# Performance work log

Hardware: AMD Instinct MI355X
Metric: run time of the kernel (lower is better)

## Reference

```python
import jax, jax.numpy as jnp
import numpy as np


def setup_inputs() -> dict:
    key = jax.random.key(0)
    ks = jax.random.split(key, 18)
    B, T, L, C = 16, 512, 50, 7
    H = 512
    s = 0.05
    inp = {
        "phone_data": jax.random.normal(ks[0], (B, T, L, C), jnp.float32),
        "h0": jax.random.normal(ks[1], (B, H), jnp.float32),
        "conv1_w": jax.random.normal(ks[2], (128, 7, 11), jnp.float32) * s,
        "conv1_b": jax.random.normal(ks[3], (128,), jnp.float32) * s,
        "conv2_w": jax.random.normal(ks[4], (256, 128, 9), jnp.float32) * s,
        "conv2_b": jax.random.normal(ks[5], (256,), jnp.float32) * s,
        "fc1_w": jax.random.normal(ks[6], (1024, 1536), jnp.float32) * s,
        "fc1_b": jax.random.normal(ks[7], (1024,), jnp.float32) * s,
        "fc2_w": jax.random.normal(ks[8], (512, 1024), jnp.float32) * s,
        "fc2_b": jax.random.normal(ks[9], (512,), jnp.float32) * s,
        "gru_wih": jax.random.normal(ks[10], (3 * H, H), jnp.float32) * s,
        "gru_whh": jax.random.normal(ks[11], (3 * H, H), jnp.float32) * s,
        "gru_bih": jax.random.normal(ks[12], (3 * H,), jnp.float32) * s,
        "gru_bhh": jax.random.normal(ks[13], (3 * H,), jnp.float32) * s,
        "fc3_w": jax.random.normal(ks[14], (1, H), jnp.float32) * s,
        "fc3_b": jax.random.normal(ks[15], (1,), jnp.float32) * s,
    }
    return inp


def reference(phone_data, h0, conv1_w, conv1_b, conv2_w, conv2_b,
              fc1_w, fc1_b, fc2_w, fc2_b,
              gru_wih, gru_whh, gru_bih, gru_bhh, fc3_w, fc3_b):
    B, T, L, C = phone_data.shape
    N = B * T
    # ---- batched CNN + FC feature extractor (independent per frame) ----
    x = phone_data.reshape(N, L, C).transpose(0, 2, 1)  # [N, 7, 50]
    y = jax.lax.conv_general_dilated(
        x, conv1_w, (1,), 'VALID',
        dimension_numbers=('NCH', 'OIH', 'NCH')) + conv1_b[None, :, None]  # [N,128,40]
    y = y.reshape(N, 128, 20, 2).max(-1)  # maxpool k=2,s=2 -> [N,128,20]
    y = jax.lax.conv_general_dilated(
        y, conv2_w, (1,), 'VALID',
        dimension_numbers=('NCH', 'OIH', 'NCH')) + conv2_b[None, :, None]  # [N,256,12]
    y = y.reshape(N, 256, 6, 2).max(-1)  # [N,256,6]
    feat = y.reshape(N, 1536)            # Flatten(0): channel-major, matches torch
    feat = feat @ fc1_w.T + fc1_b        # [N,1024]
    feat = feat @ fc2_w.T + fc2_b        # [N,512]
    feat = feat.reshape(B, T, 512)

    # ---- sequential GRUCell recurrence (PyTorch GRUCell math) ----
    def cell(h, x_t):
        gi = x_t @ gru_wih.T + gru_bih   # [B, 3H]
        gh = h @ gru_whh.T + gru_bhh     # [B, 3H]
        ir, iz, in_ = jnp.split(gi, 3, axis=-1)
        hr, hz, hn = jnp.split(gh, 3, axis=-1)
        r = jax.nn.sigmoid(ir + hr)
        z = jax.nn.sigmoid(iz + hz)
        n = jnp.tanh(in_ + r * hn)
        h_new = (1 - z) * n + z * h
        # original code calls hx.detach() every step
        h_new = jax.lax.stop_gradient(h_new)
        return h_new, h_new

    _, hs = jax.lax.scan(cell, h0, feat.transpose(1, 0, 2))  # hs: [T,B,512]
    out = hs @ fc3_w.T + fc3_b  # [T,B,1]
    return out.transpose(1, 0, 2)  # [B,T,1]
```

## Files before the change

### kernel.cpp

```cpp
#include <hip/hip_runtime.h>
#include <hip/hip_bf16.h>
#include <math.h>
#include <stdint.h>

typedef __attribute__((ext_vector_type(8))) short short8;
typedef __attribute__((ext_vector_type(4))) float f32x4;
typedef __attribute__((ext_vector_type(4))) unsigned int uint4v;

#define T_ 512

__device__ __forceinline__ unsigned short bf16rn(float f) {
  union { float f; unsigned u; } x; x.f = f;
  unsigned r = x.u + 0x7FFF + ((x.u >> 16) & 1);
  return (unsigned short)(r >> 16);
}

__device__ __forceinline__ void gload16(const void* gsrc, void* ldst) {
  __builtin_amdgcn_global_load_lds(
      (const __attribute__((address_space(1))) unsigned int*)gsrc,
      (__attribute__((address_space(3))) unsigned int*)ldst, 16, 0, 0);
}

__device__ __forceinline__ void wg_barrier() {
  __builtin_amdgcn_sched_barrier(0);
  asm volatile("s_waitcnt lgkmcnt(0)" ::: "memory");
  __builtin_amdgcn_sched_barrier(0);
  __builtin_amdgcn_s_barrier();
  __builtin_amdgcn_sched_barrier(0);
}

__global__ __launch_bounds__(256) void conv1_kernel(
    const float* __restrict__ phone, const float* __restrict__ w1,
    const float* __restrict__ b1, ushort* __restrict__ out1b) {
  __shared__ float ws[128 * 77];
  __shared__ float bs[128];
  __shared__ float xs[8][7][52];
  const int tid = threadIdx.x;
  const int n0 = blockIdx.x * 8;
  for (int idx = tid; idx < 9856; idx += 256) ws[idx] = w1[idx];
  if (tid < 128) bs[tid] = b1[tid];
  for (int idx = tid; idx < 2800; idx += 256) {
    int fi = idx / 350, r = idx - fi * 350;
    int ll = r / 7, c = r - ll * 7;
    xs[fi][c][ll] = phone[(size_t)(n0 + fi) * 350 + r];
  }
  __syncthreads();

  const int o = tid >> 1, ph = tid & 1;
  const float* wo = ws + o * 77;
  const float bb = bs[o];
  for (int fi = 0; fi < 8; ++fi) {
    float acc0[10], acc1[10];
#pragma unroll
    for (int q = 0; q < 10; ++q) { acc0[q] = 0.f; acc1[q] = 0.f; }
    for (int i = 0; i < 7; ++i) {
      float wr[11];
#pragma unroll
      for (int k = 0; k < 11; ++k) wr[k] = wo[i * 11 + k];
#pragma unroll
      for (int q = 0; q < 10; ++q) {
        int p = ph * 10 + q;
        int base = 2 * p;
        float xv[12];
#pragma unroll
        for (int j = 0; j < 12; ++j) xv[j] = xs[fi][i][base + j];
        float s0 = 0.f, s1 = 0.f;
#pragma unroll
        for (int k = 0; k < 11; ++k) {
          s0 += xv[k] * wr[k];
          s1 += xv[k + 1] * wr[k];
        }
        acc0[q] += s0;
        acc1[q] += s1;
      }
    }
#pragma unroll
    for (int q = 0; q < 10; ++q) {
      int p = ph * 10 + q;
      out1b[((size_t)(n0 + fi) * 128 + o) * 20 + p] =
          bf16rn(fmaxf(acc0[q], acc1[q]) + bb);
    }
  }
}

__global__ __launch_bounds__(256) void f32_to_bf16_multi(
    const float* __restrict__ s0, ushort* __restrict__ d0,
    const float* __restrict__ s1, ushort* __restrict__ d1,
    const float* __restrict__ s2, ushort* __restrict__ d2,
    const float* __restrict__ s3, ushort* __restrict__ d3) {
  const int n0 = 73728, n1 = 393216, n2 = 131072, n3 = 196608;
  int i = blockIdx.x * 256 + threadIdx.x;
  const float* s; ushort* d; int off;
  if (i < n0) { s = s0; d = d0; off = i; }
  else if (i < n0 + n1) { s = s1; d = d1; off = i - n0; }
  else if (i < n0 + n1 + n2) { s = s2; d = d2; off = i - n0 - n1; }
  else if (i < n0 + n1 + n2 + n3) { s = s3; d = d3; off = i - n0 - n1 - n2; }
  else return;
  float4 v = ((const float4*)s)[off];
  ushort4 o;
  o.x = bf16rn(v.x); o.y = bf16rn(v.y); o.z = bf16rn(v.z); o.w = bf16rn(v.w);
  ((ushort4*)d)[off] = o;
}

__global__ __launch_bounds__(256) void stage_h0(
    const float* __restrict__ h0, unsigned long long* __restrict__ hxt) {
  const int tid = threadIdx.x;
#pragma unroll
  for (int k = 0; k < 16; ++k) {
    int idx = tid + k * 256;
    int g = idx >> 10, rem = idx & 1023;
    int s = rem >> 6, w = rem & 63;
    int b4 = (w >> 2) & 3, fqk = w >> 4, p2 = w & 3;
    int b = g * 4 + b4;
    int D = s * 32 + fqk * 8 + p2 * 2;
    float2 h2 = *(const float2*)(h0 + (size_t)b * 512 + D);
    unsigned pk = (unsigned)bf16rn(h2.x) | ((unsigned)bf16rn(h2.y) << 16);
    hxt[(size_t)g * 2048 + rem] = (unsigned long long)pk;
  }
}

template <int AM, int EM>
__global__ __launch_bounds__(256) void gemm_bf16(
    const ushort* __restrict__ A, const ushort* __restrict__ W,
    const float* __restrict__ bias, void* __restrict__ Cout,
    int K, int lda, int ldc) {
  __shared__ ushort As[128 * 64];
  __shared__ ushort Bs[128 * 64];
  __shared__ ushort tbl[1152];
  const int tid = threadIdx.x;
  const int l = tid & 63, wv = tid >> 6;
  const int wr = wv >> 1, wc = wv & 1;
  const int fr = l & 15, fq = l >> 4;
  const int bm0 = blockIdx.x * 128, bn0 = blockIdx.y * 128;

  if (AM == 1) {
    for (int idx = tid; idx < 1152; idx += 256) {
      int i2 = idx / 9, kp = idx - i2 * 9;
      tbl[idx] = (ushort)(i2 * 20 + kp);
    }
    __syncthreads();
  }

  f32x4 acc[4][4];
#pragma unroll
  for (int mi = 0; mi < 4; ++mi)
#pragma unroll
    for (int ni = 0; ni < 4; ++ni) acc[mi][ni] = (f32x4)0.f;

  const int pr8 = l >> 3;
  const int pc = l & 7;
  const int nkt = K >> 6;
  for (int kt = 0; kt < nkt; ++kt) {
    const int k0 = kt << 6;
#pragma unroll
    for (int i = 0; i < 4; ++i) {
      int q = wv * 4 + i;
      int prow = q * 8 + pr8;
      int lc = pc ^ (prow & 7);
      gload16(W + (size_t)(bn0 + prow) * K + k0 + lc * 8, &Bs[q * 512]);
    }
    if (AM == 0) {
#pragma unroll
      for (int i = 0; i < 4; ++i) {
        int q = wv * 4 + i;
        int prow = q * 8 + pr8;
        int lc = pc ^ (prow & 7);
        gload16(A + (size_t)(bm0 + prow) * lda + k0 + lc * 8, &As[q * 512]);
      }
    } else {
#pragma unroll
      for (int q = 0; q < 16; ++q) {
        int idx = tid + q * 256;
        int row = idx >> 5, c0 = (idx & 31) * 2;
        int m = bm0 + row;
        int n = m / 12, pos = m - n * 12;
        int kk = k0 + c0;
        const ushort* an = A + (size_t)n * 2560 + pos;
        uint e0 = an[tbl[kk]];
        uint e1 = an[tbl[kk + 1]];
        *(uint*)&As[row * 64 + (((c0 >> 3) ^ (row & 7)) << 3) + (c0 & 7)] =
            e0 | (e1 << 16);
      }
    }
    __syncthreads();
#pragma unroll
    for (int ks = 0; ks < 2; ++ks) {
      short8 af[4], bfr[4];
#pragma unroll
      for (int mi = 0; mi < 4; ++mi) {
        int row = wr * 64 + mi * 16 + fr;
        af[mi] = *(const short8*)&As[row * 64 + (((ks * 4 + fq) ^ (row & 7)) << 3)];
      }
#pragma unroll
      for (int ni = 0; ni < 4; ++ni) {
        int row = wc * 64 + ni * 16 + fr;
        bfr[ni] = *(const short8*)&Bs[row * 64 + (((ks * 4 + fq) ^ (row & 7)) << 3)];
      }
#pragma unroll
      for (int mi = 0; mi < 4; ++mi)
#pragma unroll
        for (int ni = 0; ni < 4; ++ni)
          acc[mi][ni] = __builtin_amdgcn_mfma_f32_16x16x32_bf16(
              af[mi], bfr[ni], acc[mi][ni], 0, 0, 0);
    }
    __syncthreads();
  }

#pragma unroll
  for (int ni = 0; ni < 4; ++ni) {
    int col = bn0 + wc * 64 + ni * 16 + fr;
    float bv = bias[col];
#pragma unroll
    for (int mi = 0; mi < 4; ++mi) {
      int mbase = bm0 + wr * 64 + mi * 16 + fq * 4;
      if (EM == 0) {
        ushort* C = (ushort*)Cout;
#pragma unroll
        for (int j = 0; j < 4; ++j)
          C[(size_t)(mbase + j) * ldc + col] = bf16rn(acc[mi][ni][j] + bv);
      } else if (EM == 1) {
        ushort* C = (ushort*)Cout;
#pragma unroll
        for (int j = 0; j < 4; j += 2) {
          int m = mbase + j;
          int n = m / 12, pos = m - n * 12;
          float v = fmaxf(acc[mi][ni][j], acc[mi][ni][j + 1]) + bv;
          C[(size_t)n * 1536 + col * 6 + (pos >> 1)] = bf16rn(v);
        }
      } else {
        float* C = (float*)Cout;
#pragma unroll
        for (int j = 0; j < 4; ++j) {
          int m = mbase + j;
          int b = m >> 9, tt = m & 511;
          C[((size_t)tt * 16 + b) * 1536 + col] = acc[mi][ni][j] + bv;
        }
      }
    }
  }
}

__global__ __launch_bounds__(512) void gru_persistent(
    const float* __restrict__ h0, const float* __restrict__ gi,
    const float* __restrict__ whh, const float* __restrict__ bhh,
    float* __restrict__ hsbuf, unsigned long long* __restrict__ hxt) {
  __shared__ float gh_lds[24 * 64];
  __shared__ unsigned afl[16 * 64 * 4];
  const int tid = threadIdx.x;
  const int g = blockIdx.x >> 2, wp = blockIdx.x & 3;
  const int l = tid & 63, v = tid >> 6;
  const int fr = l & 15, fq = l >> 4;
  unsigned long long* hxg = hxt + (size_t)g * 2048;

  for (int i = tid; i < 4096; i += 512) afl[i] = 0u;

  const int tA = 3 * v, tB = 3 * v + 1, tC = 3 * v + 2;
  const int oA = (tA >> 3) * 512 + wp * 128 + (tA & 7) * 16 + fr;
  const int oB = (tB >> 3) * 512 + wp * 128 + (tB & 7) * 16 + fr;
  const int oC = (tC >> 3) * 512 + wp * 128 + (tC & 7) * 16 + fr;
  short8 bfA[16], bfB[16], bfC[16];
#pragma unroll
  for (int s = 0; s < 16; ++s) {
    const float* pA = whh + (size_t)oA * 512 + s * 32 + fq * 8;
    const float* pB = whh + (size_t)oB * 512 + s * 32 + fq * 8;
    const float* pC = whh + (size_t)oC * 512 + s * 32 + fq * 8;
    float4 a0 = *(const float4*)pA, a1 = *(const float4*)(pA + 4);
    float4 b0 = *(const float4*)pB, b1 = *(const float4*)(pB + 4);
    float4 c0 = *(const float4*)pC, c1 = *(const float4*)(pC + 4);
    short8 x, y, z;
    x[0] = (short)bf16rn(a0.x); x[1] = (short)bf16rn(a0.y);
    x[2] = (short)bf16rn(a0.z); x[3] = (short)bf16rn(a0.w);
    x[4] = (short)bf16rn(a1.x); x[5] = (short)bf16rn(a1.y);
    x[6] = (short)bf16rn(a1.z); x[7] = (short)bf16rn(a1.w);
    y[0] = (short)bf16rn(b0.x); y[1] = (short)bf16rn(b0.y);
    y[2] = (short)bf16rn(b0.z); y[3] = (short)bf16rn(b0.w);
    y[4] = (short)bf16rn(b1.x); y[5] = (short)bf16rn(b1.y);
    y[6] = (short)bf16rn(b1.z); y[7] = (short)bf16rn(b1.w);
    z[0] = (short)bf16rn(c0.x); z[1] = (short)bf16rn(c0.y);
    z[2] = (short)bf16rn(c0.z); z[3] = (short)bf16rn(c0.w);
    z[4] = (short)bf16rn(c1.x); z[5] = (short)bf16rn(c1.y);
    z[6] = (short)bf16rn(c1.z); z[7] = (short)bf16rn(c1.w);
    bfA[s] = x; bfB[s] = y; bfC[s] = z;
  }
  const float boA = bhh[oA], boB = bhh[oB], boC = bhh[oC];

  const int b4 = tid >> 6, jp = tid & 63, jl = jp * 2;
  const bool gthr = (tid < 256);
  const bool pthr = (tid >= 256 && tid < 384);
  const int pt = tid - 256;
  const int bglob = g * 4 + (b4 & 3);
  const int jglob = wp * 128 + jl;
  float hA = 0.f, hB = 0.f;
  float giC0 = 0.f, giC1 = 0.f, giC2 = 0.f, giC3 = 0.f, giC4 = 0.f, giC5 = 0.f;
  float giN0 = 0.f, giN1 = 0.f, giN2 = 0.f, giN3 = 0.f, giN4 = 0.f, giN5 = 0.f;
  if (gthr) {
    float2 h2 = *(const float2*)(h0 + (size_t)bglob * 512 + jglob);
    hA = h2.x; hB = h2.y;
    const float* g0 = gi + (size_t)bglob * 1536 + jglob;
    float2 r0 = *(const float2*)(g0);
    float2 r1 = *(const float2*)(g0 + 512);
    float2 r2 = *(const float2*)(g0 + 1024);
    giC0 = r0.x; giC3 = r0.y; giC1 = r1.x; giC4 = r1.y; giC2 = r2.x; giC5 = r2.y;
    const float* g1 = gi + (size_t)(16 + bglob) * 1536 + jglob;
    float2 s0 = *(const float2*)(g1);
    float2 s1 = *(const float2*)(g1 + 512);
    float2 s2 = *(const float2*)(g1 + 1024);
    giN0 = s0.x; giN3 = s0.y; giN1 = s1.x; giN4 = s1.y; giN2 = s2.x; giN5 = s2.y;
  }
  __syncthreads();

  if (pthr) {
    const int ps = pt >> 3;
    const int w0 = (pt & 7) * 8;
    const unsigned long long* base = hxg + ps * 64 + w0;
    uint4v r[4];
    for (;;) {
#pragma unroll
      for (int q = 0; q < 4; ++q)
        asm volatile("global_load_dwordx4 %0, %1, off sc0 sc1"
                     : "=v"(r[q]) : "v"(base + q * 2));
      asm volatile("s_waitcnt vmcnt(0)" ::: "memory");
      __builtin_amdgcn_sched_barrier(0);
      bool ok = true;
#pragma unroll
      for (int q = 0; q < 4; ++q)
        ok = ok & (r[q].y == 0u) & (r[q].w == 0u);
      if (ok) break;
    }
#pragma unroll
    for (int q = 0; q < 4; ++q) {
      int w = w0 + 2 * q;
      int lane = ((w >> 2) & 3) | ((w >> 4) << 4);
      *(uint2*)&afl[(ps * 64 + lane) * 4 + (w & 3)] = make_uint2(r[q].x, r[q].z);
    }
  }
  wg_barrier();

  for (int t = 0; t < T_; ++t) {
    f32x4 aA = (f32x4)0.f, aB = (f32x4)0.f, aC = (f32x4)0.f;
#pragma unroll
    for (int s = 0; s < 16; ++s) {
      union { uint4v u; short8 s8; } ca;
      ca.u = *(const uint4v*)&afl[(s * 64 + l) * 4];
      aA = __builtin_amdgcn_mfma_f32_16x16x32_bf16(ca.s8, bfA[s], aA, 0, 0, 0);
      aB = __builtin_amdgcn_mfma_f32_16x16x32_bf16(ca.s8, bfB[s], aB, 0, 0, 0);
      aC = __builtin_amdgcn_mfma_f32_16x16x32_bf16(ca.s8, bfC[s], aC, 0, 0, 0);
    }
    if (fq == 0) {
#pragma unroll
      for (int j = 0; j < 4; ++j) {
        gh_lds[tA * 64 + j * 16 + fr] = aA[j] + boA;
        gh_lds[tB * 64 + j * 16 + fr] = aB[j] + boB;
        gh_lds[tC * 64 + j * 16 + fr] = aC[j] + boC;
      }
    }
    wg_barrier();

    if (gthr) {
      const int tl = jl >> 4, c = jl & 15;
      float2 rr = *(const float2*)&gh_lds[(0 + tl) * 64 + b4 * 16 + c];
      float2 zz = *(const float2*)&gh_lds[(8 + tl) * 64 + b4 * 16 + c];
      float2 nn = *(const float2*)&gh_lds[(16 + tl) * 64 + b4 * 16 + c];
      float rgA = __builtin_amdgcn_rcpf(1.f + __expf(-(giC0 + rr.x)));
      float rgB = __builtin_amdgcn_rcpf(1.f + __expf(-(giC3 + rr.y)));
      float zgA = __builtin_amdgcn_rcpf(1.f + __expf(-(giC1 + zz.x)));
      float zgB = __builtin_amdgcn_rcpf(1.f + __expf(-(giC4 + zz.y)));
      float eA = __expf(2.f * (giC2 + rgA * nn.x));
      float eB = __expf(2.f * (giC5 + rgB * nn.y));
      float ngA = 1.f - 2.f * __builtin_amdgcn_rcpf(eA + 1.f);
      float ngB = 1.f - 2.f * __builtin_amdgcn_rcpf(eB + 1.f);
      hA = (1.f - zgA) * ngA + zgA * hA;
      hB = (1.f - zgB) * ngB + zgB * hB;
      if (t + 1 < T_) {
        unsigned pk = (unsigned)bf16rn(hA) | ((unsigned)bf16rn(hB) << 16);
        unsigned long long payload =
            (unsigned long long)pk | ((unsigned long long)(unsigned)(t + 1) << 32);
        int s = wp * 4 + (jl >> 5);
        int w_i = (((jl >> 3) & 3) * 4 + b4) * 4 + ((jl & 7) >> 1);
        __hip_atomic_store(hxg + ((t + 1) & 1) * 1024 + s * 64 + w_i, payload,
                           __ATOMIC_RELAXED, __HIP_MEMORY_SCOPE_AGENT);
      }
      *(float2*)(hsbuf + ((size_t)t * 16 + bglob) * 512 + jglob) =
          make_float2(hA, hB);
      giC0 = giN0; giC1 = giN1; giC2 = giN2;
      giC3 = giN3; giC4 = giN4; giC5 = giN5;
      if (t + 2 < T_) {
        const float* gb = gi + ((size_t)(t + 2) * 16 + bglob) * 1536 + jglob;
        float2 r0 = *(const float2*)(gb);
        float2 r1 = *(const float2*)(gb + 512);
        float2 r2 = *(const float2*)(gb + 1024);
        giN0 = r0.x; giN3 = r0.y; giN1 = r1.x; giN4 = r1.y; giN2 = r2.x; giN5 = r2.y;
      }
    } else if (pthr && t + 1 < T_) {
      const int ps = pt >> 3;
      const int w0 = (pt & 7) * 8;
      const unsigned long long* base =
          hxg + ((t + 1) & 1) * 1024 + ps * 64 + w0;
      const unsigned tag = (unsigned)(t + 1);
      uint4v r[4];
      for (;;) {
#pragma unroll
        for (int q = 0; q < 4; ++q)
          asm volatile("global_load_dwordx4 %0, %1, off sc0 sc1"
                       : "=v"(r[q]) : "v"(base + q * 2));
        asm volatile("s_waitcnt vmcnt(0)" ::: "memory");
        __builtin_amdgcn_sched_barrier(0);
        bool ok = true;
#pragma unroll
        for (int q = 0; q < 4; ++q)
          ok = ok & (r[q].y == tag) & (r[q].w == tag);
        if (ok) break;
      }
#pragma unroll
      for (int q = 0; q < 4; ++q) {
        int w = w0 + 2 * q;
        int lane = ((w >> 2) & 3) | ((w >> 4) << 4);
        *(uint2*)&afl[(ps * 64 + lane) * 4 + (w & 3)] = make_uint2(r[q].x, r[q].z);
      }
    }
    wg_barrier();
  }
}

__global__ __launch_bounds__(256) void fc3_kernel(
    const float* __restrict__ hs, const float* __restrict__ w3,
    const float* __restrict__ b3, float* __restrict__ out) {
  __shared__ float w[512];
  const int tid = threadIdx.x;
  w[tid] = w3[tid];
  w[tid + 256] = w3[tid + 256];
  __syncthreads();
  const int gidx = blockIdx.x * 256 + tid;
  const int b = gidx >> 9, t = gidx & 511;
  const float4* hr = (const float4*)(hs + ((size_t)t * 16 + b) * 512);
  const float4* wr = (const float4*)w;
  float acc = 0.f;
#pragma unroll 8
  for (int kc = 0; kc < 128; ++kc) {
    float4 h = hr[kc], ww = wr[kc];
    acc += h.x * ww.x + h.y * ww.y + h.z * ww.z + h.w * ww.w;
  }
  out[gidx] = acc + b3[0];
}

extern "C" void kernel_launch(void* const* d_in, const int* in_sizes, int n_in,
                              void* d_out, int out_size, void* d_ws,
                              size_t ws_size, hipStream_t stream) {
  const float* phone = (const float*)d_in[0];
  const float* h0    = (const float*)d_in[1];
  const float* w1    = (const float*)d_in[2];
  const float* b1    = (const float*)d_in[3];
  const float* w2    = (const float*)d_in[4];
  const float* b2    = (const float*)d_in[5];
  const float* fc1w  = (const float*)d_in[6];
  const float* fc1b  = (const float*)d_in[7];
  const float* fc2w  = (const float*)d_in[8];
  const float* fc2b  = (const float*)d_in[9];
  const float* wih   = (const float*)d_in[10];
  const float* whh   = (const float*)d_in[11];
  const float* bih   = (const float*)d_in[12];
  const float* bhh   = (const float*)d_in[13];
  const float* w3    = (const float*)d_in[14];
  const float* b3    = (const float*)d_in[15];
  float* out = (float*)d_out;

  char* ws = (char*)d_ws;
  ushort* out1b = (ushort*)(ws + 0);
  ushort* feat2 = (ushort*)(ws + 41943040);
  ushort* feat3 = (ushort*)(ws + 67108864);
  ushort* feat4 = (ushort*)(ws + 83886080);
  float*  gibuf = (float*) (ws + 92274688);
  float*  hsbuf = (float*) (ws + 142606336);
  ushort* w2b   = (ushort*)(ws + 159383552);
  ushort* fc1wb = (ushort*)(ws + 159973376);
  ushort* fc2wb = (ushort*)(ws + 163119104);
  ushort* wihb  = (ushort*)(ws + 164167680);
  unsigned long long* hxt = (unsigned long long*)(ws + 67108864);

  f32_to_bf16_multi<<<3104, 256, 0, stream>>>(w2, w2b, fc1w, fc1wb,
                                              fc2w, fc2wb, wih, wihb);

  conv1_kernel<<<1024, 256, 0, stream>>>(phone, w1, b1, out1b);
  gemm_bf16<1, 1><<<dim3(768, 2), 256, 0, stream>>>(out1b, w2b, b2, feat2, 1152, 0, 0);
  gemm_bf16<0, 0><<<dim3(64, 8), 256, 0, stream>>>(feat2, fc1wb, fc1b, feat3, 1536, 1536, 1024);
  gemm_bf16<0, 0><<<dim3(64, 4), 256, 0, stream>>>(feat3, fc2wb, fc2b, feat4, 1024, 1024, 512);
  gemm_bf16<0, 2><<<dim3(64, 12), 256, 0, stream>>>(feat4, wihb, bih, gibuf, 512, 512, 1536);

  hipMemsetAsync(hxt, 0, 65536, stream);
  stage_h0<<<1, 256, 0, stream>>>(h0, hxt);
  gru_persistent<<<16, 512, 0, stream>>>(h0, gibuf, whh, bhh, hsbuf, hxt);

  fc3_kernel<<<32, 256, 0, stream>>>(hsbuf, w3, b3, out);
}
```

Baseline: 1.529 ms.

## Restructure persistent GRU: gate-aligned MFMA tiles, double-buffered LDS, one barrier per step

Each GRU block now handles 8 batches and 64 hidden units. Every wave computes the r, z and n tiles for the same hidden indices, so the gate math runs directly on MFMA accumulators. This removes the gh_lds round-trip and one workgroup barrier per timestep. The h-vector LDS buffer is double-buffered and fed by dedicated poller waves, the initial h0 is staged in-kernel so the stage_h0 launch is dropped, and the block shrinks to 384 threads. The trade-off is that half the lanes do gate work, and the cross-block exchange now spans 8 blocks per group instead of 4.

Result: slower. 1.893 ms (+23.8%).

```diff
diff --git a/kernel.cpp b/kernel.cpp
--- a/kernel.cpp
+++ b/kernel.cpp
@@ -102,23 +102,6 @@
   ((ushort4*)d)[off] = o;
 }
 
-__global__ __launch_bounds__(256) void stage_h0(
-    const float* __restrict__ h0, unsigned long long* __restrict__ hxt) {
-  const int tid = threadIdx.x;
-#pragma unroll
-  for (int k = 0; k < 16; ++k) {
-    int idx = tid + k * 256;
-    int g = idx >> 10, rem = idx & 1023;
-    int s = rem >> 6, w = rem & 63;
-    int b4 = (w >> 2) & 3, fqk = w >> 4, p2 = w & 3;
-    int b = g * 4 + b4;
-    int D = s * 32 + fqk * 8 + p2 * 2;
-    float2 h2 = *(const float2*)(h0 + (size_t)b * 512 + D);
-    unsigned pk = (unsigned)bf16rn(h2.x) | ((unsigned)bf16rn(h2.y) << 16);
-    hxt[(size_t)g * 2048 + rem] = (unsigned long long)pk;
-  }
-}
-
 template <int AM, int EM>
 __global__ __launch_bounds__(256) void gemm_bf16(
     const ushort* __restrict__ A, const ushort* __restrict__ W,
@@ -240,33 +223,75 @@
   }
 }
 
-__global__ __launch_bounds__(512) void gru_persistent(
+__global__ __launch_bounds__(384) void gru_persistent(
     const float* __restrict__ h0, const float* __restrict__ gi,
     const float* __restrict__ whh, const float* __restrict__ bhh,
     float* __restrict__ hsbuf, unsigned long long* __restrict__ hxt) {
-  __shared__ float gh_lds[24 * 64];
-  __shared__ unsigned afl[16 * 64 * 4];
+  __shared__ unsigned afl[2][4096];
   const int tid = threadIdx.x;
-  const int g = blockIdx.x >> 2, wp = blockIdx.x & 3;
+  const int g = blockIdx.x >> 3, wp = blockIdx.x & 7;
   const int l = tid & 63, v = tid >> 6;
   const int fr = l & 15, fq = l >> 4;
-  unsigned long long* hxg = hxt + (size_t)g * 2048;
-
-  for (int i = tid; i < 4096; i += 512) afl[i] = 0u;
-
-  const int tA = 3 * v, tB = 3 * v + 1, tC = 3 * v + 2;
-  const int oA = (tA >> 3) * 512 + wp * 128 + (tA & 7) * 16 + fr;
-  const int oB = (tB >> 3) * 512 + wp * 128 + (tB & 7) * 16 + fr;
-  const int oC = (tC >> 3) * 512 + wp * 128 + (tC & 7) * 16 + fr;
-  short8 bfA[16], bfB[16], bfC[16];
+  unsigned long long* hxg = hxt + (size_t)g * 4096;
+
+  for (int i = tid; i < 2048; i += 384) {
+    int s = i >> 7, w_i = i & 127;
+    int p2 = w_i & 3, idx2 = w_i >> 2;
+    int b8 = idx2 & 7, fqk = idx2 >> 3;
+    int Dd = s * 32 + fqk * 8 + p2 * 2;
+    float2 h2 = *(const float2*)(h0 + (size_t)(g * 8 + b8) * 512 + Dd);
+    unsigned pk = (unsigned)bf16rn(h2.x) | ((unsigned)bf16rn(h2.y) << 16);
+    afl[0][(s * 64 + b8 + 16 * fqk) * 4 + p2] = pk;
+  }
+
+  if (v >= 4) {
+    const int pt = tid - 256;
+    const int ps = pt >> 3;
+    const int pw0 = (pt & 7) * 2;
+    __syncthreads();
+    for (int t = 0; t < T_; ++t) {
+      if (t + 1 < T_) {
+        const unsigned long long* base =
+            hxg + (size_t)((t + 1) & 1) * 2048 + ps * 128;
+        const unsigned tag = (unsigned)(t + 1);
+        unsigned* dst = afl[(t + 1) & 1];
+        uint4v r[8];
+        for (;;) {
+#pragma unroll
+          for (int q = 0; q < 8; ++q)
+            asm volatile("global_load_dwordx4 %0, %1, off sc0 sc1"
+                         : "=v"(r[q]) : "v"(base + pw0 + q * 16));
+          asm volatile("s_waitcnt vmcnt(0)" ::: "memory");
+          __builtin_amdgcn_sched_barrier(0);
+          bool ok = true;
+#pragma unroll
+          for (int q = 0; q < 8; ++q)
+            ok = ok & (r[q].y == tag) & (r[q].w == tag);
+          if (ok) break;
+        }
+#pragma unroll
+        for (int q = 0; q < 8; ++q) {
+          int w_i = pw0 + q * 16;
+          int lane = ((w_i >> 2) & 7) + 16 * (w_i >> 5);
+          *(uint2*)&dst[(ps * 64 + lane) * 4 + (w_i & 3)] =
+              make_uint2(r[q].x, r[q].z);
+        }
+      }
+      wg_barrier();
+    }
+    return;
+  }
+
+  const int D = wp * 64 + v * 16 + fr;
+  short8 bfR[16], bfZ[16], bfN[16];
 #pragma unroll
   for (int s = 0; s < 16; ++s) {
-    const float* pA = whh + (size_t)oA * 512 + s * 32 + fq * 8;
-    const float* pB = whh + (size_t)oB * 512 + s * 32 + fq * 8;
-    const float* pC = whh + (size_t)oC * 512 + s * 32 + fq * 8;
-    float4 a0 = *(const float4*)pA, a1 = *(const float4*)(pA + 4);
-    float4 b0 = *(const float4*)pB, b1 = *(const float4*)(pB + 4);
-    float4 c0 = *(const float4*)pC, c1 = *(const float4*)(pC + 4);
+    const float* pR = whh + (size_t)(0 * 512 + D) * 512 + s * 32 + fq * 8;
+    const float* pZ = whh + (size_t)(1 * 512 + D) * 512 + s * 32 + fq * 8;
+    const float* pN = whh + (size_t)(2 * 512 + D) * 512 + s * 32 + fq * 8;
+    float4 a0 = *(const float4*)pR, a1 = *(const float4*)(pR + 4);
+    float4 b0 = *(const float4*)pZ, b1 = *(const float4*)(pZ + 4);
+    float4 c0 = *(const float4*)pN, c1 = *(const float4*)(pN + 4);
     short8 x, y, z;
     x[0] = (short)bf16rn(a0.x); x[1] = (short)bf16rn(a0.y);
     x[2] = (short)bf16rn(a0.z); x[3] = (short)bf16rn(a0.w);
@@ -280,142 +305,81 @@
     z[2] = (short)bf16rn(c0.z); z[3] = (short)bf16rn(c0.w);
     z[4] = (short)bf16rn(c1.x); z[5] = (short)bf16rn(c1.y);
     z[6] = (short)bf16rn(c1.z); z[7] = (short)bf16rn(c1.w);
-    bfA[s] = x; bfB[s] = y; bfC[s] = z;
-  }
-  const float boA = bhh[oA], boB = bhh[oB], boC = bhh[oC];
-
-  const int b4 = tid >> 6, jp = tid & 63, jl = jp * 2;
-  const bool gthr = (tid < 256);
-  const bool pthr = (tid >= 256 && tid < 384);
-  const int pt = tid - 256;
-  const int bglob = g * 4 + (b4 & 3);
-  const int jglob = wp * 128 + jl;
-  float hA = 0.f, hB = 0.f;
-  float giC0 = 0.f, giC1 = 0.f, giC2 = 0.f, giC3 = 0.f, giC4 = 0.f, giC5 = 0.f;
-  float giN0 = 0.f, giN1 = 0.f, giN2 = 0.f, giN3 = 0.f, giN4 = 0.f, giN5 = 0.f;
-  if (gthr) {
-    float2 h2 = *(const float2*)(h0 + (size_t)bglob * 512 + jglob);
-    hA = h2.x; hB = h2.y;
-    const float* g0 = gi + (size_t)bglob * 1536 + jglob;
-    float2 r0 = *(const float2*)(g0);
-    float2 r1 = *(const float2*)(g0 + 512);
-    float2 r2 = *(const float2*)(g0 + 1024);
-    giC0 = r0.x; giC3 = r0.y; giC1 = r1.x; giC4 = r1.y; giC2 = r2.x; giC5 = r2.y;
-    const float* g1 = gi + (size_t)(16 + bglob) * 1536 + jglob;
-    float2 s0 = *(const float2*)(g1);
-    float2 s1 = *(const float2*)(g1 + 512);
-    float2 s2 = *(const float2*)(g1 + 1024);
-    giN0 = s0.x; giN3 = s0.y; giN1 = s1.x; giN4 = s1.y; giN2 = s2.x; giN5 = s2.y;
+    bfR[s] = x; bfZ[s] = y; bfN[s] = z;
+  }
+  const float boR = bhh[D], boZ = bhh[512 + D], boN = bhh[1024 + D];
+
+  const bool glane = (fq < 2);
+  float h[4];
+  float gR[4], gZ[4], gN_[4], nR[4], nZ[4], nN_[4];
+  if (glane) {
+#pragma unroll
+    for (int j = 0; j < 4; ++j) {
+      int bg = g * 8 + fq * 4 + j;
+      h[j] = h0[(size_t)bg * 512 + D];
+      const float* p0 = gi + (size_t)bg * 1536 + D;
+      gR[j] = p0[0]; gZ[j] = p0[512]; gN_[j] = p0[1024];
+      const float* p1 = gi + (size_t)(16 + bg) * 1536 + D;
+      nR[j] = p1[0]; nZ[j] = p1[512]; nN_[j] = p1[1024];
+    }
   }
   __syncthreads();
 
-  if (pthr) {
-    const int ps = pt >> 3;
-    const int w0 = (pt & 7) * 8;
-    const unsigned long long* base = hxg + ps * 64 + w0;
-    uint4v r[4];
-    for (;;) {
-#pragma unroll
-      for (int q = 0; q < 4; ++q)
-        asm volatile("global_load_dwordx4 %0, %1, off sc0 sc1"
-                     : "=v"(r[q]) : "v"(base + q * 2));
-      asm volatile("s_waitcnt vmcnt(0)" ::: "memory");
-      __builtin_amdgcn_sched_barrier(0);
-      bool ok = true;
-#pragma unroll
-      for (int q = 0; q < 4; ++q)
-        ok = ok & (r[q].y == 0u) & (r[q].w == 0u);
-      if (ok) break;
-    }
-#pragma unroll
-    for (int q = 0; q < 4; ++q) {
-      int w = w0 + 2 * q;
-      int lane = ((w >> 2) & 3) | ((w >> 4) << 4);
-      *(uint2*)&afl[(ps * 64 + lane) * 4 + (w & 3)] = make_uint2(r[q].x, r[q].z);
-    }
-  }
-  wg_barrier();
+  const int s_f = D >> 5;
+  const int wbase = (((D >> 3) & 3) * 8 + fq * 4) * 4 + ((D & 7) >> 1);
 
   for (int t = 0; t < T_; ++t) {
-    f32x4 aA = (f32x4)0.f, aB = (f32x4)0.f, aC = (f32x4)0.f;
+    const unsigned* ab = afl[t & 1];
+    f32x4 aR = (f32x4)0.f, aZ = (f32x4)0.f, aN = (f32x4)0.f;
 #pragma unroll
     for (int s = 0; s < 16; ++s) {
       union { uint4v u; short8 s8; } ca;
-      ca.u = *(const uint4v*)&afl[(s * 64 + l) * 4];
-      aA = __builtin_amdgcn_mfma_f32_16x16x32_bf16(ca.s8, bfA[s], aA, 0, 0, 0);
-      aB = __builtin_amdgcn_mfma_f32_16x16x32_bf16(ca.s8, bfB[s], aB, 0, 0, 0);
-      aC = __builtin_amdgcn_mfma_f32_16x16x32_bf16(ca.s8, bfC[s], aC, 0, 0, 0);
-    }
-    if (fq == 0) {
+      ca.u = *(const uint4v*)&ab[(s * 64 + l) * 4];
+      aR = __builtin_amdgcn_mfma_f32_16x16x32_bf16(ca.s8, bfR[s], aR, 0, 0, 0);
+      aZ = __builtin_amdgcn_mfma_f32_16x16x32_bf16(ca.s8, bfZ[s], aZ, 0, 0, 0);
+      aN = __builtin_amdgcn_mfma_f32_16x16x32_bf16(ca.s8, bfN[s], aN, 0, 0, 0);
+    }
+    if (glane) {
+      unsigned myh[4];
 #pragma unroll
       for (int j = 0; j < 4; ++j) {
-        gh_lds[tA * 64 + j * 16 + fr] = aA[j] + boA;
-        gh_lds[tB * 64 + j * 16 + fr] = aB[j] + boB;
-        gh_lds[tC * 64 + j * 16 + fr] = aC[j] + boC;
-      }
-    }
-    wg_barrier();
-
-    if (gthr) {
-      const int tl = jl >> 4, c = jl & 15;
-      float2 rr = *(const float2*)&gh_lds[(0 + tl) * 64 + b4 * 16 + c];
-      float2 zz = *(const float2*)&gh_lds[(8 + tl) * 64 + b4 * 16 + c];
-      float2 nn = *(const float2*)&gh_lds[(16 + tl) * 64 + b4 * 16 + c];
-      float rgA = __builtin_amdgcn_rcpf(1.f + __expf(-(giC0 + rr.x)));
-      float rgB = __builtin_amdgcn_rcpf(1.f + __expf(-(giC3 + rr.y)));
-      float zgA = __builtin_amdgcn_rcpf(1.f + __expf(-(giC1 + zz.x)));
-      float zgB = __builtin_amdgcn_rcpf(1.f + __expf(-(giC4 + zz.y)));
-      float eA = __expf(2.f * (giC2 + rgA * nn.x));
-      float eB = __expf(2.f * (giC5 + rgB * nn.y));
-      float ngA = 1.f - 2.f * __builtin_amdgcn_rcpf(eA + 1.f);
-      float ngB = 1.f - 2.f * __builtin_amdgcn_rcpf(eB + 1.f);
-      hA = (1.f - zgA) * ngA + zgA * hA;
-      hB = (1.f - zgB) * ngB + zgB * hB;
+        float rr = aR[j] + boR, zz = aZ[j] + boZ, nn = aN[j] + boN;
+        float rg = __builtin_amdgcn_rcpf(1.f + __expf(-(gR[j] + rr)));
+        float zg = __builtin_amdgcn_rcpf(1.f + __expf(-(gZ[j] + zz)));
+        float e = __expf(2.f * (gN_[j] + rg * nn));
+        float ng = 1.f - 2.f * __builtin_amdgcn_rcpf(e + 1.f);
+        h[j] = (1.f - zg) * ng + zg * h[j];
+        myh[j] = (unsigned)bf16rn(h[j]);
+      }
       if (t + 1 < T_) {
-        unsigned pk = (unsigned)bf16rn(hA) | ((unsigned)bf16rn(hB) << 16);
-        unsigned long long payload =
-            (unsigned long long)pk | ((unsigned long long)(unsigned)(t + 1) << 32);
-        int s = wp * 4 + (jl >> 5);
-        int w_i = (((jl >> 3) & 3) * 4 + b4) * 4 + ((jl & 7) >> 1);
-        __hip_atomic_store(hxg + ((t + 1) & 1) * 1024 + s * 64 + w_i, payload,
-                           __ATOMIC_RELAXED, __HIP_MEMORY_SCOPE_AGENT);
-      }
-      *(float2*)(hsbuf + ((size_t)t * 16 + bglob) * 512 + jglob) =
-          make_float2(hA, hB);
-      giC0 = giN0; giC1 = giN1; giC2 = giN2;
-      giC3 = giN3; giC4 = giN4; giC5 = giN5;
+        const unsigned tagw = (unsigned)(t + 1);
+        unsigned long long* pbase = hxg + (size_t)((t + 1) & 1) * 2048 + s_f * 128;
+#pragma unroll
+        for (int j = 0; j < 4; ++j) {
+          unsigned prt = (unsigned)__shfl_xor((int)myh[j], 1);
+          if ((fr & 1) == 0) {
+            unsigned pk = myh[j] | (prt << 16);
+            unsigned long long payload =
+                (unsigned long long)pk | ((unsigned long long)tagw << 32);
+            __hip_atomic_store(pbase + wbase + j * 4, payload,
+                               __ATOMIC_RELAXED, __HIP_MEMORY_SCOPE_AGENT);
+          }
+        }
+      }
+#pragma unroll
+      for (int j = 0; j < 4; ++j)
+        hsbuf[((size_t)t * 16 + g * 8 + fq * 4 + j) * 512 + D] = h[j];
+#pragma unroll
+      for (int j = 0; j < 4; ++j) {
+        gR[j] = nR[j]; gZ[j] = nZ[j]; gN_[j] = nN_[j];
+      }
       if (t + 2 < T_) {
-        const float* gb = gi + ((size_t)(t + 2) * 16 + bglob) * 1536 + jglob;
-        float2 r0 = *(const float2*)(gb);
-        float2 r1 = *(const float2*)(gb + 512);
-        float2 r2 = *(const float2*)(gb + 1024);
-        giN0 = r0.x; giN3 = r0.y; giN1 = r1.x; giN4 = r1.y; giN2 = r2.x; giN5 = r2.y;
-      }
-    } else if (pthr && t + 1 < T_) {
-      const int ps = pt >> 3;
-      const int w0 = (pt & 7) * 8;
-      const unsigned long long* base =
-          hxg + ((t + 1) & 1) * 1024 + ps * 64 + w0;
-      const unsigned tag = (unsigned)(t + 1);
-      uint4v r[4];
-      for (;;) {
-#pragma unroll
-        for (int q = 0; q < 4; ++q)
-          asm volatile("global_load_dwordx4 %0, %1, off sc0 sc1"
-                       : "=v"(r[q]) : "v"(base + q * 2));
-        asm volatile("s_waitcnt vmcnt(0)" ::: "memory");
-        __builtin_amdgcn_sched_barrier(0);
-        bool ok = true;
-#pragma unroll
-        for (int q = 0; q < 4; ++q)
-          ok = ok & (r[q].y == tag) & (r[q].w == tag);
-        if (ok) break;
-      }
-#pragma unroll
-      for (int q = 0; q < 4; ++q) {
-        int w = w0 + 2 * q;
-        int lane = ((w >> 2) & 3) | ((w >> 4) << 4);
-        *(uint2*)&afl[(ps * 64 + lane) * 4 + (w & 3)] = make_uint2(r[q].x, r[q].z);
+#pragma unroll
+        for (int j = 0; j < 4; ++j) {
+          int bg = g * 8 + fq * 4 + j;
+          const float* p = gi + ((size_t)(t + 2) * 16 + bg) * 1536 + D;
+          nR[j] = p[0]; nZ[j] = p[512]; nN_[j] = p[1024];
+        }
       }
     }
     wg_barrier();
@@ -487,8 +451,7 @@
   gemm_bf16<0, 2><<<dim3(64, 12), 256, 0, stream>>>(feat4, wihb, bih, gibuf, 512, 512, 1536);
 
   hipMemsetAsync(hxt, 0, 65536, stream);
-  stage_h0<<<1, 256, 0, stream>>>(h0, hxt);
-  gru_persistent<<<16, 512, 0, stream>>>(h0, gibuf, whh, bhh, hsbuf, hxt);
+  gru_persistent<<<16, 384, 0, stream>>>(h0, gibuf, whh, bhh, hsbuf, hxt);
 
   fc3_kernel<<<32, 256, 0, stream>>>(hsbuf, w3, b3, out);
 }
```
